# Performance work log

Measured on AMD Instinct MI355X. Metric: run time of the kernel, lower is better.

## Reference

```python
import jax, jax.numpy as jnp
import numpy as np

B, C, H, W = 8, 64, 512, 512
NUM_S = 256
EPS = 1e-7

# 3x3 neighborhood offsets excluding the center (row-major order, matching
# torch.cat([f[:, :, :4], f[:, :, 5:]], 2) after flatten of the 3x3 patch)
_DH = jnp.array([0, 0, 0, 1, 1, 2, 2, 2])
_DW = jnp.array([0, 1, 2, 0, 2, 0, 1, 2])


def setup_inputs() -> dict:
    key = jax.random.key(0)
    k1, k2, k3 = jax.random.split(key, 3)
    feat_q = jax.random.normal(k1, (B, C, H, W), dtype=jnp.float32)
    feat_k = jax.random.normal(k2, (B, C, H, W), dtype=jnp.float32)
    # h_id, w_id in [0, H-3] inclusive -> randint upper bound H-2 = 510
    sample_ids = jax.random.randint(k3, (NUM_S, 2), 0, H - 2)
    return {"feat_q": feat_q, "feat_k": feat_k, "sample_ids": sample_ids}


def _neighbor_sample(feat, sample_ids):
    # feat: [b, c, h, w]; sample_ids: [num_s, 2]
    b, c, h, w = feat.shape
    hi = sample_ids[:, 0]
    wi = sample_ids[:, 1]
    # gather 8 neighbors per sampled location: [b, c, num_s, 8]
    nb = feat[:, :, hi[:, None] + _DH[None, :], wi[:, None] + _DW[None, :]]
    # center pixel: [b, c, num_s, 1]
    ctr = feat[:, :, hi + 1, wi + 1][:, :, :, None]
    ft = (nb - ctr).reshape(b, c, -1)  # [b, c, 8*num_s]
    # L2 normalize over channel dim (Normalize(power=2) with eps=1e-7)
    norm = jnp.sqrt(jnp.sum(ft * ft, axis=1, keepdims=True))
    return ft / (norm + EPS)


def reference(feat_q, feat_k, sample_ids):
    f_q = _neighbor_sample(feat_q, sample_ids)
    f_k = _neighbor_sample(feat_k, sample_ids)
    # L1Loss with default mean reduction; single layer (num_l=1)
    return jnp.mean(jnp.abs(f_q - f_k))
```

## Files before the change

kernel.cpp:

```cpp
#include <hip/hip_runtime.h>
#include <hip/hip_bf16.h>

#define NUM_SAMPLES 256
#define CH 64
#define IMG_H 512
#define IMG_W 512
#define BATCH 8

__device__ __forceinline__ float wave_reduce_sum(float v) {
    v += __shfl_xor(v, 32, 64);
    v += __shfl_xor(v, 16, 64);
    v += __shfl_xor(v, 8, 64);
    v += __shfl_xor(v, 4, 64);
    v += __shfl_xor(v, 2, 64);
    v += __shfl_xor(v, 1, 64);
    return v;
}

__global__ void __launch_bounds__(64)
sample_diff_kernel(const float* __restrict__ fq,
                   const float* __restrict__ fk,
                   const int* __restrict__ ids,
                   float* __restrict__ partial) {
    const int c  = threadIdx.x;
    const int bs = blockIdx.x;
    const int b  = bs >> 8;
    const int s  = bs & (NUM_SAMPLES - 1);

    const int hi = ids[2 * s + 0];
    const int wi = ids[2 * s + 1];

    const size_t HW   = (size_t)IMG_H * IMG_W;
    const size_t base = ((size_t)(b * CH + c)) * HW + (size_t)hi * IMG_W + wi;

    float qv[9], kv[9];
#pragma unroll
    for (int r = 0; r < 3; ++r) {
#pragma unroll
        for (int col = 0; col < 3; ++col) {
            qv[r * 3 + col] = fq[base + (size_t)r * IMG_W + col];
            kv[r * 3 + col] = fk[base + (size_t)r * IMG_W + col];
        }
    }

    const float qc = qv[4];
    const float kc = kv[4];

    const int nidx[8] = {0, 1, 2, 3, 5, 6, 7, 8};

    float dq[8], dk[8];
#pragma unroll
    for (int n = 0; n < 8; ++n) {
        dq[n] = qv[nidx[n]] - qc;
        dk[n] = kv[nidx[n]] - kc;
    }

    float rnq[8], rnk[8];
#pragma unroll
    for (int n = 0; n < 8; ++n) {
        const float sq = wave_reduce_sum(dq[n] * dq[n]);
        const float sk = wave_reduce_sum(dk[n] * dk[n]);
        rnq[n] = 1.0f / (sqrtf(sq) + 1e-7f);
        rnk[n] = 1.0f / (sqrtf(sk) + 1e-7f);
    }

    float acc = 0.0f;
#pragma unroll
    for (int n = 0; n < 8; ++n)
        acc += fabsf(dq[n] * rnq[n] - dk[n] * rnk[n]);

    acc = wave_reduce_sum(acc);
    if (c == 0) partial[bs] = acc;
}

__global__ void __launch_bounds__(256)
final_reduce_kernel(const float* __restrict__ partial, float* __restrict__ out) {
    __shared__ float sm[4];
    const int t = threadIdx.x;
    float v = 0.0f;
    for (int i = t; i < BATCH * NUM_SAMPLES; i += 256)
        v += partial[i];
    v = wave_reduce_sum(v);
    if ((t & 63) == 0) sm[t >> 6] = v;
    __syncthreads();
    if (t == 0) {
        const float tot = sm[0] + sm[1] + sm[2] + sm[3];
        out[0] = tot * (1.0f / 1048576.0f);
    }
}

extern "C" void kernel_launch(void* const* d_in, const int* in_sizes, int n_in,
                              void* d_out, int out_size, void* d_ws, size_t ws_size,
                              hipStream_t stream) {
    const float* fq  = (const float*)d_in[0];
    const float* fk  = (const float*)d_in[1];
    const int*   ids = (const int*)d_in[2];
    float* out     = (float*)d_out;
    float* partial = (float*)d_ws;

    sample_diff_kernel<<<BATCH * NUM_SAMPLES, 64, 0, stream>>>(fq, fk, ids, partial);
    final_reduce_kernel<<<1, 256, 0, stream>>>(partial, out);
}
```

Baseline: 32.32 us.

## Split gather into separate kernel staging neighbor diffs in workspace

Adds a gather kernel where each thread handles one sample for a fixed (batch, channel) plane. It loads the 3x3 patch as three 3-float row reads per tensor and writes the 8 q and 8 k differences as float4s to a workspace buffer. The norm kernel then reads these contiguous float4s per channel and does the channel-wise L2 normalization and L1 accumulation, and the final reduce is vectorized. The aim is better memory parallelism for the scattered gather, at the cost of an extra kernel launch and a round trip of about 8 MB through the workspace.

After: 31.41 us. 1.03x faster.

```diff
diff --git a/kernel.cpp b/kernel.cpp
--- a/kernel.cpp
+++ b/kernel.cpp
@@ -3,9 +3,12 @@
 
 #define NUM_SAMPLES 256
 #define CH 64
-#define IMG_H 512
 #define IMG_W 512
 #define BATCH 8
+#define NBLOCKS (BATCH * NUM_SAMPLES)
+#define HW ((size_t)512 * 512)
+
+struct F3 { float x, y, z; };
 
 __device__ __forceinline__ float wave_reduce_sum(float v) {
     v += __shfl_xor(v, 32, 64);
@@ -17,58 +20,54 @@
     return v;
 }
 
+__global__ void __launch_bounds__(256)
+gather_kernel(const float* __restrict__ fq, const float* __restrict__ fk,
+              const int* __restrict__ ids, float* __restrict__ wsd) {
+    const int bc = blockIdx.x;
+    const int s  = threadIdx.x;
+    const int hi = ids[2 * s + 0];
+    const int wi = ids[2 * s + 1];
+    const size_t base = (size_t)bc * HW + (size_t)hi * IMG_W + wi;
+
+    const F3 q0 = *(const F3*)(fq + base);
+    const F3 q1 = *(const F3*)(fq + base + IMG_W);
+    const F3 q2 = *(const F3*)(fq + base + 2 * IMG_W);
+    const F3 k0 = *(const F3*)(fk + base);
+    const F3 k1 = *(const F3*)(fk + base + IMG_W);
+    const F3 k2 = *(const F3*)(fk + base + 2 * IMG_W);
+
+    const float qc = q1.y, kc = k1.y;
+    const float4 o0 = make_float4(q0.x - qc, q0.y - qc, q0.z - qc, q1.x - qc);
+    const float4 o1 = make_float4(q1.z - qc, q2.x - qc, q2.y - qc, q2.z - qc);
+    const float4 o2 = make_float4(k0.x - kc, k0.y - kc, k0.z - kc, k1.x - kc);
+    const float4 o3 = make_float4(k1.z - kc, k2.x - kc, k2.y - kc, k2.z - kc);
+
+    float4* dst = (float4*)wsd + ((size_t)bc * NUM_SAMPLES + s) * 4;
+    dst[0] = o0; dst[1] = o1; dst[2] = o2; dst[3] = o3;
+}
+
 __global__ void __launch_bounds__(64)
-sample_diff_kernel(const float* __restrict__ fq,
-                   const float* __restrict__ fk,
-                   const int* __restrict__ ids,
-                   float* __restrict__ partial) {
+norm_kernel(const float* __restrict__ wsd, float* __restrict__ partial) {
     const int c  = threadIdx.x;
     const int bs = blockIdx.x;
     const int b  = bs >> 8;
     const int s  = bs & (NUM_SAMPLES - 1);
 
-    const int hi = ids[2 * s + 0];
-    const int wi = ids[2 * s + 1];
-
-    const size_t HW   = (size_t)IMG_H * IMG_W;
-    const size_t base = ((size_t)(b * CH + c)) * HW + (size_t)hi * IMG_W + wi;
-
-    float qv[9], kv[9];
-#pragma unroll
-    for (int r = 0; r < 3; ++r) {
-#pragma unroll
-        for (int col = 0; col < 3; ++col) {
-            qv[r * 3 + col] = fq[base + (size_t)r * IMG_W + col];
-            kv[r * 3 + col] = fk[base + (size_t)r * IMG_W + col];
-        }
-    }
-
-    const float qc = qv[4];
-    const float kc = kv[4];
-
-    const int nidx[8] = {0, 1, 2, 3, 5, 6, 7, 8};
-
-    float dq[8], dk[8];
-#pragma unroll
-    for (int n = 0; n < 8; ++n) {
-        dq[n] = qv[nidx[n]] - qc;
-        dk[n] = kv[nidx[n]] - kc;
-    }
-
-    float rnq[8], rnk[8];
-#pragma unroll
-    for (int n = 0; n < 8; ++n) {
-        const float sq = wave_reduce_sum(dq[n] * dq[n]);
-        const float sk = wave_reduce_sum(dk[n] * dk[n]);
-        rnq[n] = 1.0f / (sqrtf(sq) + 1e-7f);
-        rnk[n] = 1.0f / (sqrtf(sk) + 1e-7f);
-    }
+    const float4* src =
+        (const float4*)wsd + ((size_t)(b * CH + c) * NUM_SAMPLES + s) * 4;
+    const float4 a0 = src[0], a1 = src[1], a2 = src[2], a3 = src[3];
+    const float qd[8] = {a0.x, a0.y, a0.z, a0.w, a1.x, a1.y, a1.z, a1.w};
+    const float kd[8] = {a2.x, a2.y, a2.z, a2.w, a3.x, a3.y, a3.z, a3.w};
 
     float acc = 0.0f;
 #pragma unroll
-    for (int n = 0; n < 8; ++n)
-        acc += fabsf(dq[n] * rnq[n] - dk[n] * rnk[n]);
-
+    for (int n = 0; n < 8; ++n) {
+        const float sq = wave_reduce_sum(qd[n] * qd[n]);
+        const float sk = wave_reduce_sum(kd[n] * kd[n]);
+        const float qn = qd[n] * (1.0f / (sqrtf(sq) + 1e-7f));
+        const float kn = kd[n] * (1.0f / (sqrtf(sk) + 1e-7f));
+        acc += fabsf(qn - kn);
+    }
     acc = wave_reduce_sum(acc);
     if (c == 0) partial[bs] = acc;
 }
@@ -77,9 +76,9 @@
 final_reduce_kernel(const float* __restrict__ partial, float* __restrict__ out) {
     __shared__ float sm[4];
     const int t = threadIdx.x;
-    float v = 0.0f;
-    for (int i = t; i < BATCH * NUM_SAMPLES; i += 256)
-        v += partial[i];
+    const float4 v0 = ((const float4*)partial)[t * 2 + 0];
+    const float4 v1 = ((const float4*)partial)[t * 2 + 1];
+    float v = v0.x + v0.y + v0.z + v0.w + v1.x + v1.y + v1.z + v1.w;
     v = wave_reduce_sum(v);
     if ((t & 63) == 0) sm[t >> 6] = v;
     __syncthreads();
@@ -96,8 +95,10 @@
     const float* fk  = (const float*)d_in[1];
     const int*   ids = (const int*)d_in[2];
     float* out     = (float*)d_out;
-    float* partial = (float*)d_ws;
+    float* wsd     = (float*)d_ws;
+    float* partial = (float*)d_ws + (size_t)BATCH * CH * NUM_SAMPLES * 16;
 
-    sample_diff_kernel<<<BATCH * NUM_SAMPLES, 64, 0, stream>>>(fq, fk, ids, partial);
+    gather_kernel<<<BATCH * CH, NUM_SAMPLES, 0, stream>>>(fq, fk, ids, wsd);
+    norm_kernel<<<NBLOCKS, 64, 0, stream>>>(wsd, partial);
     final_reduce_kernel<<<1, 256, 0, stream>>>(partial, out);
 }
```
